# Kernel optimization log

Measured on AMD Instinct MI355X. Metric: run time of the kernel, lower is better.

Reference implementation:

```python
import jax, jax.numpy as jnp
import numpy as np

N = 100000
E = 1200000
F_IN = 64
H = 64
C = 10


def _gcn_norm(edge_idx):
    # PyG gcn_norm with add_self_loops=True, edge_weight=1
    src = jnp.concatenate([edge_idx[0], jnp.arange(N, dtype=edge_idx.dtype)])
    dst = jnp.concatenate([edge_idx[1], jnp.arange(N, dtype=edge_idx.dtype)])
    deg = jax.ops.segment_sum(jnp.ones_like(dst, dtype=jnp.float32), dst, num_segments=N)
    dinv = jnp.where(deg > 0, jax.lax.rsqrt(deg), 0.0)
    norm = dinv[src] * dinv[dst]  # [E+N]
    return src, dst, norm


def _gcn_conv(x, src, dst, norm, W, b):
    h = x @ W                               # [N, out]
    msg = h[src] * norm[:, None]            # gather + scale, [E+N, out]
    out = jax.ops.segment_sum(msg, dst, num_segments=N)  # scatter-add
    return out + b


def setup_inputs() -> dict:
    key = jax.random.key(0)
    ks = jax.random.split(key, 8)
    x = jax.random.normal(ks[0], (N, F_IN), dtype=jnp.float32)
    edge_idx = jax.random.randint(ks[1], (2, E), 0, N, dtype=jnp.int64 if jax.config.jax_enable_x64 else jnp.int32)
    def glorot(k, fan_in, fan_out):
        s = jnp.sqrt(6.0 / (fan_in + fan_out)).astype(jnp.float32)
        return jax.random.uniform(k, (fan_in, fan_out), jnp.float32, -s, s)
    W0 = glorot(ks[2], F_IN, H); b0 = jnp.zeros((H,), jnp.float32)
    W1 = glorot(ks[3], H, H);    b1 = jnp.zeros((H,), jnp.float32)
    W2 = glorot(ks[4], H, H);    b2 = jnp.zeros((H,), jnp.float32)
    Wl = glorot(ks[5], H, C);    bl = jnp.zeros((C,), jnp.float32)
    return {"x": x, "edge_idx": edge_idx, "W0": W0, "b0": b0,
            "W1": W1, "b1": b1, "W2": W2, "b2": b2, "Wl": Wl, "bl": bl}


def reference(x, edge_idx, W0, b0, W1, b1, W2, b2, Wl, bl):
    src, dst, norm = _gcn_norm(edge_idx)
    # conv0 + relu
    h = jax.nn.relu(_gcn_conv(x, src, dst, norm, W0, b0))
    # convs[0] + relu (i=0 < num_layers-2=1)
    h = jax.nn.relu(_gcn_conv(h, src, dst, norm, W1, b1))
    # convs[1], no relu (last)
    h = _gcn_conv(h, src, dst, norm, W2, b2)
    # global_add_pool(batch=None): sum over all nodes, keepdim -> [1, H]
    g = jnp.sum(h, axis=0, keepdims=True)
    # dropout is identity in eval mode
    return g @ Wl + bl  # [1, C]
```

## Files before the change

### kernel.cpp

```cpp
#include <hip/hip_runtime.h>
#include <hip/hip_bf16.h>

#define NN 100000
#define NE 1200000
#define NE4 (NE / 4)
#define XCD_N 8
#define NPX (NN / XCD_N)
#define CAP 64
#define SPILL_MAX 4096

__global__ __launch_bounds__(256) void bucket_fill_kernel(const int* __restrict__ esrc,
                                                          const int* __restrict__ edst,
                                                          int* __restrict__ deg,
                                                          int* __restrict__ bucket,
                                                          int* __restrict__ spill,
                                                          int* __restrict__ spill_cnt) {
    int xcd = blockIdx.x & 7;
    int sub = blockIdx.x >> 3;
    int nsub = gridDim.x >> 3;
    int lo = xcd * NPX;
    for (int i = sub * 256 + threadIdx.x; i < NE4; i += nsub * 256) {
        int4 d  = ((const int4*)edst)[i];
        int4 sr = ((const int4*)esrc)[i];
        #pragma unroll
        for (int c = 0; c < 4; ++c) {
            int dd = (c == 0) ? d.x : (c == 1) ? d.y : (c == 2) ? d.z : d.w;
            int ss = (c == 0) ? sr.x : (c == 1) ? sr.y : (c == 2) ? sr.z : sr.w;
            if ((unsigned)(dd - lo) < NPX) {
                int slot = atomicAdd(&deg[dd], 1);
                if (slot < CAP) {
                    bucket[dd * CAP + slot] = ss;
                } else {
                    int p = atomicAdd(spill_cnt, 1);
                    if (p < SPILL_MAX) { spill[2 * p] = dd; spill[2 * p + 1] = ss; }
                }
            }
        }
    }
}

__global__ __launch_bounds__(256) void dinv_kernel(const int* __restrict__ deg,
                                                   float* __restrict__ dinv) {
    int n = blockIdx.x * 256 + threadIdx.x;
    if (n < NN) dinv[n] = rsqrtf((float)(deg[n] + 1));
}

template <int MODE>
__global__ __launch_bounds__(256) void mm_kernel(const void* __restrict__ in,
                                                 const float* __restrict__ W,
                                                 const float* __restrict__ bias,
                                                 const float* __restrict__ dinv,
                                                 __hip_bfloat16* __restrict__ u) {
    __shared__ float Ws[64 * 64];
    __shared__ float hrow[4][64];
    int tid = threadIdx.x;
    {
        const float4* Wv = (const float4*)W;
        float4* Wsv = (float4*)Ws;
        #pragma unroll
        for (int i = 0; i < 4; ++i) Wsv[tid + 256 * i] = Wv[tid + 256 * i];
    }
    int local = tid >> 6;
    int f = tid & 63;
    int n = blockIdx.x * 4 + local;
    float din = dinv[n];
    float v;
    if (MODE == 0) {
        v = ((const float*)in)[n * 64 + f];
    } else {
        v = __bfloat162float(((const __hip_bfloat16*)in)[n * 64 + f]);
        v = fmaxf(fmaf(din, v, bias[f]), 0.f);
    }
    hrow[local][f] = v;
    __syncthreads();
    float acc = 0.f;
    #pragma unroll
    for (int k = 0; k < 64; ++k)
        acc = fmaf(hrow[local][k], Ws[k * 64 + f], acc);
    u[n * 64 + f] = __float2bfloat16(din * acc);
}

__device__ __forceinline__ void acc_bf8(float acc[8], uint4 v) {
    acc[0] += __uint_as_float(v.x << 16);
    acc[1] += __uint_as_float(v.x & 0xffff0000u);
    acc[2] += __uint_as_float(v.y << 16);
    acc[3] += __uint_as_float(v.y & 0xffff0000u);
    acc[4] += __uint_as_float(v.z << 16);
    acc[5] += __uint_as_float(v.z & 0xffff0000u);
    acc[6] += __uint_as_float(v.w << 16);
    acc[7] += __uint_as_float(v.w & 0xffff0000u);
}

__device__ __forceinline__ unsigned packbf2(float lof, float hif) {
    __hip_bfloat16 l = __float2bfloat16(lof), h = __float2bfloat16(hif);
    unsigned short ul, uh;
    __builtin_memcpy(&ul, &l, 2);
    __builtin_memcpy(&uh, &h, 2);
    return ((unsigned)uh << 16) | ul;
}

__device__ __forceinline__ void agg_row(const int* __restrict__ degv,
                                        const int* __restrict__ bucket,
                                        const uint4* __restrict__ u4,
                                        const int* __restrict__ spill,
                                        const int* __restrict__ spill_cnt,
                                        int n, int lane, int grp, int fo,
                                        float acc[8]) {
    float acc2[8];
    #pragma unroll
    for (int i = 0; i < 8; ++i) { acc[i] = 0.f; acc2[i] = 0.f; }
    int deg = degv[n];
    int dc = deg < CAP ? deg : CAP;
    int cidx = -1;
    if (lane < dc) cidx = bucket[n * CAP + lane];
    if (grp == 0) acc_bf8(acc, u4[n * 8 + fo]);
    int s0 = __shfl(cidx, grp);
    int s1 = __shfl(cidx, grp + 8);
    if (grp < dc) acc_bf8(acc, u4[s0 * 8 + fo]);
    if (grp + 8 < dc) acc_bf8(acc2, u4[s1 * 8 + fo]);
    for (int j = grp + 16; j < dc; j += 8) {
        int s = __shfl(cidx, j);
        acc_bf8(acc, u4[s * 8 + fo]);
    }
    if (deg > CAP) {
        int cnt = *spill_cnt; if (cnt > SPILL_MAX) cnt = SPILL_MAX;
        for (int e = 0; e < cnt; ++e) {
            if (spill[2 * e] == n && grp == 0)
                acc_bf8(acc2, u4[spill[2 * e + 1] * 8 + fo]);
        }
    }
    #pragma unroll
    for (int i = 0; i < 8; ++i) {
        float v = acc[i] + acc2[i];
        v += __shfl_xor(v, 8);
        v += __shfl_xor(v, 16);
        v += __shfl_xor(v, 32);
        acc[i] = v;
    }
}

template <int POOL>
__global__ __launch_bounds__(256, 8) void agg_kernel(const int* __restrict__ degv,
                                                     const int* __restrict__ bucket,
                                                     const uint4* __restrict__ uin,
                                                     const float* __restrict__ dinv,
                                                     const int* __restrict__ spill,
                                                     const int* __restrict__ spill_cnt,
                                                     __hip_bfloat16* __restrict__ a,
                                                     float* __restrict__ gp) {
    __shared__ float gpart[64];
    int tid = threadIdx.x;
    if (POOL) {
        if (tid < 64) gpart[tid] = 0.f;
        __syncthreads();
    }
    int lane = tid & 63;
    int grp = lane >> 3;
    int fo = lane & 7;
    int n = blockIdx.x * 4 + (tid >> 6);
    float acc[8];
    agg_row(degv, bucket, uin, spill, spill_cnt, n, lane, grp, fo, acc);
    if (POOL) {
        if (grp == 0) {
            float din = dinv[n];
            #pragma unroll
            for (int i = 0; i < 8; ++i) atomicAdd(&gpart[fo * 8 + i], din * acc[i]);
        }
        __syncthreads();
        if (tid < 64) atomicAdd(&gp[(blockIdx.x & 63) * 64 + tid], gpart[tid]);
    } else {
        if (grp == 0) {
            uint4 pv;
            pv.x = packbf2(acc[0], acc[1]);
            pv.y = packbf2(acc[2], acc[3]);
            pv.z = packbf2(acc[4], acc[5]);
            pv.w = packbf2(acc[6], acc[7]);
            ((uint4*)a)[n * 8 + fo] = pv;
        }
    }
}

__global__ __launch_bounds__(64) void head_kernel(const float* __restrict__ gp,
                                                  const float* __restrict__ b2,
                                                  const float* __restrict__ Wl,
                                                  const float* __restrict__ bl,
                                                  float* __restrict__ out) {
    int t = threadIdx.x;
    float s = 0.f;
    #pragma unroll 8
    for (int r = 0; r < 64; ++r) s += gp[r * 64 + t];
    float gf = s + (float)NN * b2[t];
    #pragma unroll
    for (int c = 0; c < 10; ++c) {
        float p = gf * Wl[t * 10 + c];
        #pragma unroll
        for (int off = 32; off > 0; off >>= 1) p += __shfl_down(p, off);
        if (t == 0) out[c] = p + bl[c];
    }
}

extern "C" void kernel_launch(void* const* d_in, const int* in_sizes, int n_in,
                              void* d_out, int out_size, void* d_ws, size_t ws_size,
                              hipStream_t stream) {
    const float* x  = (const float*)d_in[0];
    const int* eidx = (const int*)d_in[1];
    const int* esrc = eidx;
    const int* edst = eidx + NE;
    const float* W0 = (const float*)d_in[2];
    const float* b0 = (const float*)d_in[3];
    const float* W1 = (const float*)d_in[4];
    const float* b1 = (const float*)d_in[5];
    const float* W2 = (const float*)d_in[6];
    const float* b2 = (const float*)d_in[7];
    const float* Wl = (const float*)d_in[8];
    const float* bl = (const float*)d_in[9];
    float* out = (float*)d_out;

    float* ws = (float*)d_ws;
    size_t off = 0;
    int*   deg    = (int*)(ws + off); off += NN;
    float* dinv   =        ws + off;  off += NN;
    __hip_bfloat16* u = (__hip_bfloat16*)(ws + off); off += (size_t)NN * 32;
    __hip_bfloat16* a = (__hip_bfloat16*)(ws + off); off += (size_t)NN * 32;
    float* gp     =        ws + off;  off += 64 * 64;
    int*   spill_cnt = (int*)(ws + off); off += 4;
    int*   spill  = (int*)(ws + off); off += 2 * SPILL_MAX;
    int*   bucket = (int*)(ws + off); off += (size_t)NN * CAP;

    hipMemsetAsync(deg, 0, NN * sizeof(int), stream);
    hipMemsetAsync(gp, 0, (64 * 64 + 4) * sizeof(float), stream);

    bucket_fill_kernel<<<2048, 256, 0, stream>>>(esrc, edst, deg, bucket, spill, spill_cnt);
    dinv_kernel<<<(NN + 255) / 256, 256, 0, stream>>>(deg, dinv);

    mm_kernel<0><<<NN / 4, 256, 0, stream>>>(x, W0, nullptr, dinv, u);
    agg_kernel<0><<<NN / 4, 256, 0, stream>>>(deg, bucket, (const uint4*)u, dinv, spill, spill_cnt, a, gp);
    mm_kernel<1><<<NN / 4, 256, 0, stream>>>(a, W1, b0, dinv, u);
    agg_kernel<0><<<NN / 4, 256, 0, stream>>>(deg, bucket, (const uint4*)u, dinv, spill, spill_cnt, a, gp);
    mm_kernel<1><<<NN / 4, 256, 0, stream>>>(a, W2, b1, dinv, u);
    agg_kernel<1><<<NN / 4, 256, 0, stream>>>(deg, bucket, (const uint4*)u, dinv, spill, spill_cnt, a, gp);
    head_kernel<<<1, 64, 0, stream>>>(gp, b2, Wl, bl, out);
}
```

Measured before the change: 345.6 us.

## Fuse aggregation with next-layer matmul and compute dinv inline

Merges each aggregation pass with the following layer's dense transform (bias, ReLU, 64x64 matmul) into one kernel, so the intermediate aggregated bf16 tensor is never written to or re-read from global memory. It also drops the separate dinv kernel and buffer, recomputing rsqrt of degree inline. Together these remove three kernel launches and one round trip of a 100000x64 bf16 array per layer. In exchange, each fused block must load the full 64x64 weight matrix into shared memory and uses more registers and LDS, so the occupancy hint drops from 8 to 6 blocks per CU.

```diff
diff --git a/kernel.cpp b/kernel.cpp
--- a/kernel.cpp
+++ b/kernel.cpp
@@ -39,18 +39,10 @@
     }
 }
 
-__global__ __launch_bounds__(256) void dinv_kernel(const int* __restrict__ deg,
-                                                   float* __restrict__ dinv) {
-    int n = blockIdx.x * 256 + threadIdx.x;
-    if (n < NN) dinv[n] = rsqrtf((float)(deg[n] + 1));
-}
-
-template <int MODE>
-__global__ __launch_bounds__(256) void mm_kernel(const void* __restrict__ in,
-                                                 const float* __restrict__ W,
-                                                 const float* __restrict__ bias,
-                                                 const float* __restrict__ dinv,
-                                                 __hip_bfloat16* __restrict__ u) {
+__global__ __launch_bounds__(256) void mm0_kernel(const float* __restrict__ in,
+                                                  const float* __restrict__ W,
+                                                  const int* __restrict__ deg,
+                                                  __hip_bfloat16* __restrict__ u) {
     __shared__ float Ws[64 * 64];
     __shared__ float hrow[4][64];
     int tid = threadIdx.x;
@@ -63,15 +55,8 @@
     int local = tid >> 6;
     int f = tid & 63;
     int n = blockIdx.x * 4 + local;
-    float din = dinv[n];
-    float v;
-    if (MODE == 0) {
-        v = ((const float*)in)[n * 64 + f];
-    } else {
-        v = __bfloat162float(((const __hip_bfloat16*)in)[n * 64 + f]);
-        v = fmaxf(fmaf(din, v, bias[f]), 0.f);
-    }
-    hrow[local][f] = v;
+    float din = rsqrtf((float)(deg[n] + 1));
+    hrow[local][f] = in[n * 64 + f];
     __syncthreads();
     float acc = 0.f;
     #pragma unroll
@@ -89,14 +74,6 @@
     acc[5] += __uint_as_float(v.z & 0xffff0000u);
     acc[6] += __uint_as_float(v.w << 16);
     acc[7] += __uint_as_float(v.w & 0xffff0000u);
-}
-
-__device__ __forceinline__ unsigned packbf2(float lof, float hif) {
-    __hip_bfloat16 l = __float2bfloat16(lof), h = __float2bfloat16(hif);
-    unsigned short ul, uh;
-    __builtin_memcpy(&ul, &l, 2);
-    __builtin_memcpy(&uh, &h, 2);
-    return ((unsigned)uh << 16) | ul;
 }
 
 __device__ __forceinline__ void agg_row(const int* __restrict__ degv,
@@ -139,45 +116,84 @@
     }
 }
 
-template <int POOL>
-__global__ __launch_bounds__(256, 8) void agg_kernel(const int* __restrict__ degv,
-                                                     const int* __restrict__ bucket,
-                                                     const uint4* __restrict__ uin,
-                                                     const float* __restrict__ dinv,
-                                                     const int* __restrict__ spill,
-                                                     const int* __restrict__ spill_cnt,
-                                                     __hip_bfloat16* __restrict__ a,
-                                                     float* __restrict__ gp) {
+__global__ __launch_bounds__(256, 6) void aggmm_kernel(const int* __restrict__ degv,
+                                                       const int* __restrict__ bucket,
+                                                       const uint4* __restrict__ uin,
+                                                       const int* __restrict__ spill,
+                                                       const int* __restrict__ spill_cnt,
+                                                       const float* __restrict__ bias,
+                                                       const float* __restrict__ W,
+                                                       __hip_bfloat16* __restrict__ uout) {
+    __shared__ float Ws[64 * 64];
+    __shared__ float hrow[4][64];
+    int tid = threadIdx.x;
+    {
+        const float4* Wv = (const float4*)W;
+        float4* Wsv = (float4*)Ws;
+        #pragma unroll
+        for (int i = 0; i < 4; ++i) Wsv[tid + 256 * i] = Wv[tid + 256 * i];
+    }
+    __syncthreads();
+    int wid = tid >> 6;
+    int lane = tid & 63;
+    int grp = lane >> 3;
+    int fo = lane & 7;
+    int n = blockIdx.x * 4 + wid;
+    float acc[8];
+    agg_row(degv, bucket, uin, spill, spill_cnt, n, lane, grp, fo, acc);
+    float din = rsqrtf((float)(degv[n] + 1));
+    if (grp == 0) {
+        float4 blo = ((const float4*)bias)[fo * 2];
+        float4 bhi = ((const float4*)bias)[fo * 2 + 1];
+        float4 lo, hi;
+        lo.x = fmaxf(fmaf(din, acc[0], blo.x), 0.f);
+        lo.y = fmaxf(fmaf(din, acc[1], blo.y), 0.f);
+        lo.z = fmaxf(fmaf(din, acc[2], blo.z), 0.f);
+        lo.w = fmaxf(fmaf(din, acc[3], blo.w), 0.f);
+        hi.x = fmaxf(fmaf(din, acc[4], bhi.x), 0.f);
+        hi.y = fmaxf(fmaf(din, acc[5], bhi.y), 0.f);
+        hi.z = fmaxf(fmaf(din, acc[6], bhi.z), 0.f);
+        hi.w = fmaxf(fmaf(din, acc[7], bhi.w), 0.f);
+        ((float4*)hrow[wid])[fo * 2] = lo;
+        ((float4*)hrow[wid])[fo * 2 + 1] = hi;
+    }
+    float o = 0.f;
+    const float4* hv = (const float4*)hrow[wid];
+    #pragma unroll
+    for (int k4 = 0; k4 < 16; ++k4) {
+        float4 h = hv[k4];
+        int kb = k4 * 4;
+        o = fmaf(h.x, Ws[(kb + 0) * 64 + lane], o);
+        o = fmaf(h.y, Ws[(kb + 1) * 64 + lane], o);
+        o = fmaf(h.z, Ws[(kb + 2) * 64 + lane], o);
+        o = fmaf(h.w, Ws[(kb + 3) * 64 + lane], o);
+    }
+    uout[n * 64 + lane] = __float2bfloat16(din * o);
+}
+
+__global__ __launch_bounds__(256, 6) void aggpool_kernel(const int* __restrict__ degv,
+                                                         const int* __restrict__ bucket,
+                                                         const uint4* __restrict__ uin,
+                                                         const int* __restrict__ spill,
+                                                         const int* __restrict__ spill_cnt,
+                                                         float* __restrict__ gp) {
     __shared__ float gpart[64];
     int tid = threadIdx.x;
-    if (POOL) {
-        if (tid < 64) gpart[tid] = 0.f;
-        __syncthreads();
-    }
+    if (tid < 64) gpart[tid] = 0.f;
+    __syncthreads();
     int lane = tid & 63;
     int grp = lane >> 3;
     int fo = lane & 7;
     int n = blockIdx.x * 4 + (tid >> 6);
     float acc[8];
     agg_row(degv, bucket, uin, spill, spill_cnt, n, lane, grp, fo, acc);
-    if (POOL) {
-        if (grp == 0) {
-            float din = dinv[n];
-            #pragma unroll
-            for (int i = 0; i < 8; ++i) atomicAdd(&gpart[fo * 8 + i], din * acc[i]);
-        }
-        __syncthreads();
-        if (tid < 64) atomicAdd(&gp[(blockIdx.x & 63) * 64 + tid], gpart[tid]);
-    } else {
-        if (grp == 0) {
-            uint4 pv;
-            pv.x = packbf2(acc[0], acc[1]);
-            pv.y = packbf2(acc[2], acc[3]);
-            pv.z = packbf2(acc[4], acc[5]);
-            pv.w = packbf2(acc[6], acc[7]);
-            ((uint4*)a)[n * 8 + fo] = pv;
-        }
-    }
+    if (grp == 0) {
+        float din = rsqrtf((float)(degv[n] + 1));
+        #pragma unroll
+        for (int i = 0; i < 8; ++i) atomicAdd(&gpart[fo * 8 + i], din * acc[i]);
+    }
+    __syncthreads();
+    if (tid < 64) atomicAdd(&gp[(blockIdx.x & 63) * 64 + tid], gpart[tid]);
 }
 
 __global__ __launch_bounds__(64) void head_kernel(const float* __restrict__ gp,
@@ -219,9 +235,8 @@
     float* ws = (float*)d_ws;
     size_t off = 0;
     int*   deg    = (int*)(ws + off); off += NN;
-    float* dinv   =        ws + off;  off += NN;
-    __hip_bfloat16* u = (__hip_bfloat16*)(ws + off); off += (size_t)NN * 32;
-    __hip_bfloat16* a = (__hip_bfloat16*)(ws + off); off += (size_t)NN * 32;
+    __hip_bfloat16* ua = (__hip_bfloat16*)(ws + off); off += (size_t)NN * 32;
+    __hip_bfloat16* ub = (__hip_bfloat16*)(ws + off); off += (size_t)NN * 32;
     float* gp     =        ws + off;  off += 64 * 64;
     int*   spill_cnt = (int*)(ws + off); off += 4;
     int*   spill  = (int*)(ws + off); off += 2 * SPILL_MAX;
@@ -231,13 +246,10 @@
     hipMemsetAsync(gp, 0, (64 * 64 + 4) * sizeof(float), stream);
 
     bucket_fill_kernel<<<2048, 256, 0, stream>>>(esrc, edst, deg, bucket, spill, spill_cnt);
-    dinv_kernel<<<(NN + 255) / 256, 256, 0, stream>>>(deg, dinv);
-
-    mm_kernel<0><<<NN / 4, 256, 0, stream>>>(x, W0, nullptr, dinv, u);
-    agg_kernel<0><<<NN / 4, 256, 0, stream>>>(deg, bucket, (const uint4*)u, dinv, spill, spill_cnt, a, gp);
-    mm_kernel<1><<<NN / 4, 256, 0, stream>>>(a, W1, b0, dinv, u);
-    agg_kernel<0><<<NN / 4, 256, 0, stream>>>(deg, bucket, (const uint4*)u, dinv, spill, spill_cnt, a, gp);
-    mm_kernel<1><<<NN / 4, 256, 0, stream>>>(a, W2, b1, dinv, u);
-    agg_kernel<1><<<NN / 4, 256, 0, stream>>>(deg, bucket, (const uint4*)u, dinv, spill, spill_cnt, a, gp);
+
+    mm0_kernel<<<NN / 4, 256, 0, stream>>>(x, W0, deg, ua);
+    aggmm_kernel<<<NN / 4, 256, 0, stream>>>(deg, bucket, (const uint4*)ua, spill, spill_cnt, b0, W1, ub);
+    aggmm_kernel<<<NN / 4, 256, 0, stream>>>(deg, bucket, (const uint4*)ub, spill, spill_cnt, b1, W2, ua);
+    aggpool_kernel<<<NN / 4, 256, 0, stream>>>(deg, bucket, (const uint4*)ua, spill, spill_cnt, gp);
     head_kernel<<<1, 64, 0, stream>>>(gp, b2, Wl, bl, out);
 }
```

Result: faster. 333.5 us (-3.5%).

## Split features into two halves by XCD and inline dinv computation

Applied to the files above, without the earlier changes.

Stores the transformed features as two separate 32-wide bf16 halves and maps aggregation blocks so that blocks 0-3 of each group of eight (by block index) read the low half and blocks 4-7 read the high half. This is meant to halve the gather working set each XCD touches, so it fits better in per-XCD L2. The dinv kernel is removed and rsqrt(deg+1) is computed inline wherever it is needed. The cost is twice as many aggregation blocks and redundant neighbor-index loads, since each half re-reads the bucket lists.

```diff
diff --git a/kernel.cpp b/kernel.cpp
--- a/kernel.cpp
+++ b/kernel.cpp
@@ -8,6 +8,7 @@
 #define NPX (NN / XCD_N)
 #define CAP 64
 #define SPILL_MAX 4096
+#define AGG_GRID 50000
 
 __global__ __launch_bounds__(256) void bucket_fill_kernel(const int* __restrict__ esrc,
                                                           const int* __restrict__ edst,
@@ -39,18 +40,13 @@
     }
 }
 
-__global__ __launch_bounds__(256) void dinv_kernel(const int* __restrict__ deg,
-                                                   float* __restrict__ dinv) {
-    int n = blockIdx.x * 256 + threadIdx.x;
-    if (n < NN) dinv[n] = rsqrtf((float)(deg[n] + 1));
-}
-
 template <int MODE>
 __global__ __launch_bounds__(256) void mm_kernel(const void* __restrict__ in,
                                                  const float* __restrict__ W,
                                                  const float* __restrict__ bias,
-                                                 const float* __restrict__ dinv,
-                                                 __hip_bfloat16* __restrict__ u) {
+                                                 const int* __restrict__ deg,
+                                                 __hip_bfloat16* __restrict__ ul,
+                                                 __hip_bfloat16* __restrict__ uh) {
     __shared__ float Ws[64 * 64];
     __shared__ float hrow[4][64];
     int tid = threadIdx.x;
@@ -63,7 +59,7 @@
     int local = tid >> 6;
     int f = tid & 63;
     int n = blockIdx.x * 4 + local;
-    float din = dinv[n];
+    float din = rsqrtf((float)(deg[n] + 1));
     float v;
     if (MODE == 0) {
         v = ((const float*)in)[n * 64 + f];
@@ -77,60 +73,58 @@
     #pragma unroll
     for (int k = 0; k < 64; ++k)
         acc = fmaf(hrow[local][k], Ws[k * 64 + f], acc);
-    u[n * 64 + f] = __float2bfloat16(din * acc);
-}
-
-__device__ __forceinline__ void acc_bf8(float acc[8], uint4 v) {
+    __hip_bfloat16 r = __float2bfloat16(din * acc);
+    if (f < 32) ul[n * 32 + f] = r;
+    else        uh[n * 32 + (f - 32)] = r;
+}
+
+__device__ __forceinline__ void acc_bf4(float acc[4], uint2 v) {
     acc[0] += __uint_as_float(v.x << 16);
     acc[1] += __uint_as_float(v.x & 0xffff0000u);
     acc[2] += __uint_as_float(v.y << 16);
     acc[3] += __uint_as_float(v.y & 0xffff0000u);
-    acc[4] += __uint_as_float(v.z << 16);
-    acc[5] += __uint_as_float(v.z & 0xffff0000u);
-    acc[6] += __uint_as_float(v.w << 16);
-    acc[7] += __uint_as_float(v.w & 0xffff0000u);
 }
 
 __device__ __forceinline__ unsigned packbf2(float lof, float hif) {
     __hip_bfloat16 l = __float2bfloat16(lof), h = __float2bfloat16(hif);
-    unsigned short ul, uh;
-    __builtin_memcpy(&ul, &l, 2);
-    __builtin_memcpy(&uh, &h, 2);
-    return ((unsigned)uh << 16) | ul;
-}
-
-__device__ __forceinline__ void agg_row(const int* __restrict__ degv,
-                                        const int* __restrict__ bucket,
-                                        const uint4* __restrict__ u4,
-                                        const int* __restrict__ spill,
-                                        const int* __restrict__ spill_cnt,
-                                        int n, int lane, int grp, int fo,
-                                        float acc[8]) {
-    float acc2[8];
-    #pragma unroll
-    for (int i = 0; i < 8; ++i) { acc[i] = 0.f; acc2[i] = 0.f; }
+    unsigned short ull, uhh;
+    __builtin_memcpy(&ull, &l, 2);
+    __builtin_memcpy(&uhh, &h, 2);
+    return ((unsigned)uhh << 16) | ull;
+}
+
+__device__ __forceinline__ void agg_row_half(const int* __restrict__ degv,
+                                             const int* __restrict__ bucket,
+                                             const uint2* __restrict__ u2,
+                                             const int* __restrict__ spill,
+                                             const int* __restrict__ spill_cnt,
+                                             int n, int lane, int grp, int fo,
+                                             float acc[4]) {
+    float acc2[4];
+    #pragma unroll
+    for (int i = 0; i < 4; ++i) { acc[i] = 0.f; acc2[i] = 0.f; }
     int deg = degv[n];
     int dc = deg < CAP ? deg : CAP;
     int cidx = -1;
     if (lane < dc) cidx = bucket[n * CAP + lane];
-    if (grp == 0) acc_bf8(acc, u4[n * 8 + fo]);
+    if (grp == 0) acc_bf4(acc, u2[n * 8 + fo]);
     int s0 = __shfl(cidx, grp);
     int s1 = __shfl(cidx, grp + 8);
-    if (grp < dc) acc_bf8(acc, u4[s0 * 8 + fo]);
-    if (grp + 8 < dc) acc_bf8(acc2, u4[s1 * 8 + fo]);
+    if (grp < dc) acc_bf4(acc, u2[s0 * 8 + fo]);
+    if (grp + 8 < dc) acc_bf4(acc2, u2[s1 * 8 + fo]);
     for (int j = grp + 16; j < dc; j += 8) {
         int s = __shfl(cidx, j);
-        acc_bf8(acc, u4[s * 8 + fo]);
+        acc_bf4(acc, u2[s * 8 + fo]);
     }
     if (deg > CAP) {
         int cnt = *spill_cnt; if (cnt > SPILL_MAX) cnt = SPILL_MAX;
         for (int e = 0; e < cnt; ++e) {
             if (spill[2 * e] == n && grp == 0)
-                acc_bf8(acc2, u4[spill[2 * e + 1] * 8 + fo]);
-        }
-    }
-    #pragma unroll
-    for (int i = 0; i < 8; ++i) {
+                acc_bf4(acc2, u2[spill[2 * e + 1] * 8 + fo]);
+        }
+    }
+    #pragma unroll
+    for (int i = 0; i < 4; ++i) {
         float v = acc[i] + acc2[i];
         v += __shfl_xor(v, 8);
         v += __shfl_xor(v, 16);
@@ -142,40 +136,42 @@
 template <int POOL>
 __global__ __launch_bounds__(256, 8) void agg_kernel(const int* __restrict__ degv,
                                                      const int* __restrict__ bucket,
-                                                     const uint4* __restrict__ uin,
-                                                     const float* __restrict__ dinv,
+                                                     const uint2* __restrict__ ulv,
+                                                     const uint2* __restrict__ uhv,
                                                      const int* __restrict__ spill,
                                                      const int* __restrict__ spill_cnt,
-                                                     __hip_bfloat16* __restrict__ a,
+                                                     __hip_bfloat16* __restrict__ ah,
                                                      float* __restrict__ gp) {
-    __shared__ float gpart[64];
+    __shared__ float gpart[32];
     int tid = threadIdx.x;
     if (POOL) {
-        if (tid < 64) gpart[tid] = 0.f;
+        if (tid < 32) gpart[tid] = 0.f;
         __syncthreads();
     }
+    int k = blockIdx.x & 7;
+    int half = k >> 2;
+    int g = (blockIdx.x >> 3) * 4 + (k & 3);
+    const uint2* u2 = half ? uhv : ulv;
     int lane = tid & 63;
     int grp = lane >> 3;
     int fo = lane & 7;
-    int n = blockIdx.x * 4 + (tid >> 6);
-    float acc[8];
-    agg_row(degv, bucket, uin, spill, spill_cnt, n, lane, grp, fo, acc);
+    int n = g * 4 + (tid >> 6);
+    float acc[4];
+    agg_row_half(degv, bucket, u2, spill, spill_cnt, n, lane, grp, fo, acc);
     if (POOL) {
         if (grp == 0) {
-            float din = dinv[n];
+            float din = rsqrtf((float)(degv[n] + 1));
             #pragma unroll
-            for (int i = 0; i < 8; ++i) atomicAdd(&gpart[fo * 8 + i], din * acc[i]);
+            for (int i = 0; i < 4; ++i) atomicAdd(&gpart[fo * 4 + i], din * acc[i]);
         }
         __syncthreads();
-        if (tid < 64) atomicAdd(&gp[(blockIdx.x & 63) * 64 + tid], gpart[tid]);
+        if (tid < 32) atomicAdd(&gp[(blockIdx.x & 63) * 64 + half * 32 + tid], gpart[tid]);
     } else {
         if (grp == 0) {
-            uint4 pv;
+            uint2 pv;
             pv.x = packbf2(acc[0], acc[1]);
             pv.y = packbf2(acc[2], acc[3]);
-            pv.z = packbf2(acc[4], acc[5]);
-            pv.w = packbf2(acc[6], acc[7]);
-            ((uint4*)a)[n * 8 + fo] = pv;
+            ((uint2*)ah)[n * 16 + half * 8 + fo] = pv;
         }
     }
 }
@@ -219,9 +215,9 @@
     float* ws = (float*)d_ws;
     size_t off = 0;
     int*   deg    = (int*)(ws + off); off += NN;
-    float* dinv   =        ws + off;  off += NN;
-    __hip_bfloat16* u = (__hip_bfloat16*)(ws + off); off += (size_t)NN * 32;
-    __hip_bfloat16* a = (__hip_bfloat16*)(ws + off); off += (size_t)NN * 32;
+    __hip_bfloat16* ah = (__hip_bfloat16*)(ws + off); off += (size_t)NN * 32;
+    __hip_bfloat16* ul = (__hip_bfloat16*)(ws + off); off += (size_t)NN * 16;
+    __hip_bfloat16* uh = (__hip_bfloat16*)(ws + off); off += (size_t)NN * 16;
     float* gp     =        ws + off;  off += 64 * 64;
     int*   spill_cnt = (int*)(ws + off); off += 4;
     int*   spill  = (int*)(ws + off); off += 2 * SPILL_MAX;
@@ -231,13 +227,15 @@
     hipMemsetAsync(gp, 0, (64 * 64 + 4) * sizeof(float), stream);
 
     bucket_fill_kernel<<<2048, 256, 0, stream>>>(esrc, edst, deg, bucket, spill, spill_cnt);
-    dinv_kernel<<<(NN + 255) / 256, 256, 0, stream>>>(deg, dinv);
-
-    mm_kernel<0><<<NN / 4, 256, 0, stream>>>(x, W0, nullptr, dinv, u);
-    agg_kernel<0><<<NN / 4, 256, 0, stream>>>(deg, bucket, (const uint4*)u, dinv, spill, spill_cnt, a, gp);
-    mm_kernel<1><<<NN / 4, 256, 0, stream>>>(a, W1, b0, dinv, u);
-    agg_kernel<0><<<NN / 4, 256, 0, stream>>>(deg, bucket, (const uint4*)u, dinv, spill, spill_cnt, a, gp);
-    mm_kernel<1><<<NN / 4, 256, 0, stream>>>(a, W2, b1, dinv, u);
-    agg_kernel<1><<<NN / 4, 256, 0, stream>>>(deg, bucket, (const uint4*)u, dinv, spill, spill_cnt, a, gp);
+
+    mm_kernel<0><<<NN / 4, 256, 0, stream>>>(x, W0, nullptr, deg, ul, uh);
+    agg_kernel<0><<<AGG_GRID, 256, 0, stream>>>(deg, bucket, (const uint2*)ul, (const uint2*)uh,
+                                                spill, spill_cnt, ah, gp);
+    mm_kernel<1><<<NN / 4, 256, 0, stream>>>(ah, W1, b0, deg, ul, uh);
+    agg_kernel<0><<<AGG_GRID, 256, 0, stream>>>(deg, bucket, (const uint2*)ul, (const uint2*)uh,
+                                                spill, spill_cnt, ah, gp);
+    mm_kernel<1><<<NN / 4, 256, 0, stream>>>(ah, W2, b1, deg, ul, uh);
+    agg_kernel<1><<<AGG_GRID, 256, 0, stream>>>(deg, bucket, (const uint2*)ul, (const uint2*)uh,
+                                                spill, spill_cnt, ah, gp);
     head_kernel<<<1, 64, 0, stream>>>(gp, b2, Wl, bl, out);
 }
```

After: 399.1 us. 15.5% more time.

## Inline dinv computation and remap aggregation blocks onto half the XCDs

Applied to the files above, without the earlier changes.

Drops the separate dinv kernel and its buffer, and recomputes rsqrt(deg+1) inline in the matmul and pooling kernels, saving one launch and one pass over a small array. The aggregation grid grows to 50000 blocks, but blocks whose index mod 8 is 4 or more exit at once. The remaining blocks are remapped so all node groups are still covered, which places the gather work on only four of the eight XCDs under round-robin dispatch. The likely aim is better L2 locality for the gathered features. The risk is losing half the compute and memory parallelism in the dominant kernels.

```diff
diff --git a/kernel.cpp b/kernel.cpp
--- a/kernel.cpp
+++ b/kernel.cpp
@@ -8,6 +8,7 @@
 #define NPX (NN / XCD_N)
 #define CAP 64
 #define SPILL_MAX 4096
+#define AGG_GRID 50000
 
 __global__ __launch_bounds__(256) void bucket_fill_kernel(const int* __restrict__ esrc,
                                                           const int* __restrict__ edst,
@@ -39,17 +40,11 @@
     }
 }
 
-__global__ __launch_bounds__(256) void dinv_kernel(const int* __restrict__ deg,
-                                                   float* __restrict__ dinv) {
-    int n = blockIdx.x * 256 + threadIdx.x;
-    if (n < NN) dinv[n] = rsqrtf((float)(deg[n] + 1));
-}
-
 template <int MODE>
 __global__ __launch_bounds__(256) void mm_kernel(const void* __restrict__ in,
                                                  const float* __restrict__ W,
                                                  const float* __restrict__ bias,
-                                                 const float* __restrict__ dinv,
+                                                 const int* __restrict__ deg,
                                                  __hip_bfloat16* __restrict__ u) {
     __shared__ float Ws[64 * 64];
     __shared__ float hrow[4][64];
@@ -63,7 +58,7 @@
     int local = tid >> 6;
     int f = tid & 63;
     int n = blockIdx.x * 4 + local;
-    float din = dinv[n];
+    float din = rsqrtf((float)(deg[n] + 1));
     float v;
     if (MODE == 0) {
         v = ((const float*)in)[n * 64 + f];
@@ -143,26 +138,28 @@
 __global__ __launch_bounds__(256, 8) void agg_kernel(const int* __restrict__ degv,
                                                      const int* __restrict__ bucket,
                                                      const uint4* __restrict__ uin,
-                                                     const float* __restrict__ dinv,
                                                      const int* __restrict__ spill,
                                                      const int* __restrict__ spill_cnt,
                                                      __hip_bfloat16* __restrict__ a,
                                                      float* __restrict__ gp) {
+    int k = blockIdx.x & 7;
+    if (k >= 4) return;
     __shared__ float gpart[64];
     int tid = threadIdx.x;
     if (POOL) {
         if (tid < 64) gpart[tid] = 0.f;
         __syncthreads();
     }
+    int g = (blockIdx.x >> 3) * 4 + k;
     int lane = tid & 63;
     int grp = lane >> 3;
     int fo = lane & 7;
-    int n = blockIdx.x * 4 + (tid >> 6);
+    int n = g * 4 + (tid >> 6);
     float acc[8];
     agg_row(degv, bucket, uin, spill, spill_cnt, n, lane, grp, fo, acc);
     if (POOL) {
         if (grp == 0) {
-            float din = dinv[n];
+            float din = rsqrtf((float)(degv[n] + 1));
             #pragma unroll
             for (int i = 0; i < 8; ++i) atomicAdd(&gpart[fo * 8 + i], din * acc[i]);
         }
@@ -219,7 +216,6 @@
     float* ws = (float*)d_ws;
     size_t off = 0;
     int*   deg    = (int*)(ws + off); off += NN;
-    float* dinv   =        ws + off;  off += NN;
     __hip_bfloat16* u = (__hip_bfloat16*)(ws + off); off += (size_t)NN * 32;
     __hip_bfloat16* a = (__hip_bfloat16*)(ws + off); off += (size_t)NN * 32;
     float* gp     =        ws + off;  off += 64 * 64;
@@ -231,13 +227,12 @@
     hipMemsetAsync(gp, 0, (64 * 64 + 4) * sizeof(float), stream);
 
     bucket_fill_kernel<<<2048, 256, 0, stream>>>(esrc, edst, deg, bucket, spill, spill_cnt);
-    dinv_kernel<<<(NN + 255) / 256, 256, 0, stream>>>(deg, dinv);
-
-    mm_kernel<0><<<NN / 4, 256, 0, stream>>>(x, W0, nullptr, dinv, u);
-    agg_kernel<0><<<NN / 4, 256, 0, stream>>>(deg, bucket, (const uint4*)u, dinv, spill, spill_cnt, a, gp);
-    mm_kernel<1><<<NN / 4, 256, 0, stream>>>(a, W1, b0, dinv, u);
-    agg_kernel<0><<<NN / 4, 256, 0, stream>>>(deg, bucket, (const uint4*)u, dinv, spill, spill_cnt, a, gp);
-    mm_kernel<1><<<NN / 4, 256, 0, stream>>>(a, W2, b1, dinv, u);
-    agg_kernel<1><<<NN / 4, 256, 0, stream>>>(deg, bucket, (const uint4*)u, dinv, spill, spill_cnt, a, gp);
+
+    mm_kernel<0><<<NN / 4, 256, 0, stream>>>(x, W0, nullptr, deg, u);
+    agg_kernel<0><<<AGG_GRID, 256, 0, stream>>>(deg, bucket, (const uint4*)u, spill, spill_cnt, a, gp);
+    mm_kernel<1><<<NN / 4, 256, 0, stream>>>(a, W1, b0, deg, u);
+    agg_kernel<0><<<AGG_GRID, 256, 0, stream>>>(deg, bucket, (const uint4*)u, spill, spill_cnt, a, gp);
+    mm_kernel<1><<<NN / 4, 256, 0, stream>>>(a, W2, b1, deg, u);
+    agg_kernel<1><<<AGG_GRID, 256, 0, stream>>>(deg, bucket, (const uint4*)u, spill, spill_cnt, a, gp);
     head_kernel<<<1, 64, 0, stream>>>(gp, b2, Wl, bl, out);
 }
```

After: 464.1 us. 1.34x slower.
